# Kernel tuning notes

Hardware: AMD Instinct MI355X
Metric: run time of the kernel (lower is better)

Reference implementation:

```python
import jax, jax.numpy as jnp
import numpy as np

S = 2   # upsample scale
K = 5   # reassembly kernel k_up


def setup_inputs() -> dict:
    key = jax.random.key(0)
    ks = jax.random.split(key, 7)
    B, C, H, W = 4, 128, 64, 64
    C_MID = 64
    return {
        "x": jax.random.normal(ks[0], (B, C, H, W), dtype=jnp.float32),
        "w1": jax.random.normal(ks[1], (C_MID, C), dtype=jnp.float32) * 0.05,
        "w2": jax.random.normal(ks[2], (S * S * K * K, C_MID, 3, 3), dtype=jnp.float32) * 0.05,
        "bn_gamma": jax.random.uniform(ks[3], (C_MID,), dtype=jnp.float32, minval=0.5, maxval=1.5),
        "bn_beta": jax.random.normal(ks[4], (C_MID,), dtype=jnp.float32) * 0.1,
        "bn_mean": jax.random.normal(ks[5], (C_MID,), dtype=jnp.float32) * 0.1,
        "bn_var": jax.random.uniform(ks[6], (C_MID,), dtype=jnp.float32, minval=0.5, maxval=1.5),
    }


def reference(x, w1, w2, bn_gamma, bn_beta, bn_mean, bn_var):
    B, C, H, W = x.shape
    s, k = S, K
    eps = 1e-5
    # --- content encoder: 1x1 conv -> BN (inference form) -> ReLU -> 3x3 conv ---
    h = jnp.einsum('bchw,oc->bohw', x, w1)  # (B, c_mid, H, W)
    inv = bn_gamma / jnp.sqrt(bn_var + eps)
    h = h * inv[None, :, None, None] + (bn_beta - bn_mean * inv)[None, :, None, None]
    h = jax.nn.relu(h)
    ker = jax.lax.conv_general_dilated(
        h, w2, window_strides=(1, 1), padding=((1, 1), (1, 1)),
        dimension_numbers=('NCHW', 'OIHW', 'NCHW'))  # (B, s*s*k*k, H, W)
    # softmax over the k*k reassembly window
    ker = jax.nn.softmax(ker.reshape(B, s * s, k * k, H, W), axis=2)
    # --- unfold k x k neighborhoods of x (row-major window order, as F.unfold) ---
    p = k // 2
    xp = jnp.pad(x, ((0, 0), (0, 0), (p, p), (p, p)))
    patches = jnp.stack(
        [xp[:, :, i:i + H, j:j + W] for i in range(k) for j in range(k)],
        axis=2)  # (B, C, k*k, H, W)
    # weighted reassembly: sum over the k*k window per (sub-pixel, channel)
    out = jnp.einsum('bckhw,bskhw->bcshw', patches, ker)  # (B, C, s*s, H, W)
    # pixel shuffle: (B, C, s, s, H, W) -> (B, C, H*s, W*s)
    out = out.reshape(B, C, s, s, H, W).transpose(0, 1, 4, 2, 5, 3)
    return out.reshape(B, C, H * s, W * s)
```

## Files before the change

kernel.cpp:

```cpp
#include <hip/hip_runtime.h>
#include <hip/hip_bf16.h>

#define HW 4096

typedef __attribute__((ext_vector_type(8))) short  short8;
typedef __attribute__((ext_vector_type(4))) float  floatx4;

#define OFF_W2B 0ul
#define OFF_W1B 129024ul
#define OFF_BN  145408ul

__device__ __forceinline__ float bfbits(unsigned u) {
    union { unsigned u; float f; } t; t.u = u; return t.f;
}

__global__ __launch_bounds__(256) void prep_kernel(const float* __restrict__ w1,
                                                   const float* __restrict__ w2,
                                                   const float* __restrict__ gamma,
                                                   const float* __restrict__ beta,
                                                   const float* __restrict__ mean,
                                                   const float* __restrict__ var,
                                                   char* __restrict__ ws) {
    int tid = blockIdx.x * 256 + threadIdx.x;
    if (tid < 64512) {
        int n = tid / 576;
        int k = tid - n * 576;
        int t = k >> 6, c = k & 63;
        float v = (n < 100) ? w2[(n * 64 + c) * 9 + t] : 0.f;
        ((__hip_bfloat16*)(ws + OFF_W2B))[tid] = __float2bfloat16(v);
    } else if (tid < 64512 + 8192) {
        int i = tid - 64512;
        ((__hip_bfloat16*)(ws + OFF_W1B))[i] = __float2bfloat16(w1[i]);
    } else if (tid < 64512 + 8192 + 64) {
        int o = tid - 64512 - 8192;
        float inv = gamma[o] * rsqrtf(var[o] + 1e-5f);
        ((float2*)(ws + OFF_BN))[o] = make_float2(inv, beta[o] - mean[o] * inv);
    }
}

__global__ __launch_bounds__(1024, 8) void fused_carafe(const float* __restrict__ x,
                                                        const char* __restrict__ ws,
                                                        float* __restrict__ out) {
    __shared__ __align__(16) __hip_bfloat16 xs[96 * 136];
    __shared__ __align__(16) __hip_bfloat16 hs[60 * 72];
    __shared__ __align__(16) float lg[32 * 114];
    __shared__ __align__(16) float ks[32 * 104];

    int b    = blockIdx.x >> 7;
    int tile = blockIdx.x & 127;
    int ty0 = (tile >> 3) * 4;
    int tx0 = (tile & 7) * 8;
    int tid = threadIdx.x;
    int lane = tid & 63, wave = tid >> 6;
    int q = lane >> 4, m = lane & 15;

    int bnt = wave >> 2;
    int bo  = bnt * 16 + m;
    const __hip_bfloat16* w1b = (const __hip_bfloat16*)(ws + OFF_W1B);
    short8 bw[4];
    #pragma unroll
    for (int s = 0; s < 4; ++s)
        bw[s] = *(const short8*)(w1b + bo * 128 + s * 32 + q * 8);
    float2 bnia = ((const float2*)(ws + OFF_BN))[bo];

    const float* xb = x + (size_t)b * 128 * HW;
    #pragma unroll
    for (int i = 0; i < 12; ++i) {
        int idx = tid + i * 1024;
        int c = idx / 96, p = idx - c * 96;
        int hy = p / 12, hx = p - hy * 12;
        int gy = ty0 + hy - 2, gx = tx0 + hx - 2;
        float v = 0.f;
        if ((unsigned)gy < 64u && (unsigned)gx < 64u)
            v = xb[(size_t)c * HW + gy * 64 + gx];
        xs[p * 136 + c] = __float2bfloat16(v);
    }
    __syncthreads();

    {
        int mt = wave & 3;
        int hp = mt * 16 + m;
        int hy1 = hp / 10, hx1 = hp - hy1 * 10;
        int xrow = (hy1 + 1) * 12 + (hx1 + 1);
        floatx4 acc;
        #pragma unroll
        for (int r = 0; r < 4; ++r) acc[r] = 0.f;
        #pragma unroll
        for (int s = 0; s < 4; ++s) {
            short8 a = *(const short8*)(&xs[xrow * 136 + s * 32 + q * 8]);
            acc = __builtin_amdgcn_mfma_f32_16x16x32_bf16(a, bw[s], acc, 0, 0, 0);
        }
        #pragma unroll
        for (int r = 0; r < 4; ++r) {
            int prow = mt * 16 + q * 4 + r;
            if (prow < 60) {
                int phy = prow / 10, phx = prow - phy * 10;
                int gy = ty0 + phy - 1, gx = tx0 + phx - 1;
                bool in = ((unsigned)gy < 64u) && ((unsigned)gx < 64u);
                float v = in ? fmaxf(fmaf(acc[r], bnia.x, bnia.y), 0.f) : 0.f;
                hs[prow * 72 + bo] = __float2bfloat16(v);
            }
        }
    }
    __syncthreads();

    {
        int mt = wave & 1, nt = wave >> 1;
        if (nt < 7) {
            int pixidx = mt * 16 + m;
            int py = pixidx >> 3, px = pixidx & 7;
            const __hip_bfloat16* w2b = (const __hip_bfloat16*)(ws + OFF_W2B);
            const __hip_bfloat16* bp  = w2b + (size_t)(nt * 16 + m) * 576 + q * 8;

            floatx4 acc;
            #pragma unroll
            for (int r = 0; r < 4; ++r) acc[r] = 0.f;

            short8 bcur = *(const short8*)bp;
            for (int s = 0; s < 18; ++s) {
                int t = s >> 1, c0 = (s & 1) * 32;
                int ti = t / 3, tj = t - ti * 3;
                short8 a = *(const short8*)(&hs[((py + ti) * 10 + px + tj) * 72 + c0 + q * 8]);
                short8 bn2 = bcur;
                if (s < 17) bn2 = *(const short8*)(bp + (s + 1) * 32);
                acc = __builtin_amdgcn_mfma_f32_16x16x32_bf16(a, bcur, acc, 0, 0, 0);
                bcur = bn2;
            }
            #pragma unroll
            for (int r = 0; r < 4; ++r)
                lg[(mt * 16 + q * 4 + r) * 114 + nt * 16 + m] = acc[r];
        }
    }
    __syncthreads();

    if (tid < 128) {
        int pix = tid & 31, g = tid >> 5;
        float v[25];
        #pragma unroll
        for (int wi = 0; wi < 25; ++wi) v[wi] = lg[pix * 114 + g * 25 + wi];
        float mx = v[0];
        #pragma unroll
        for (int wi = 1; wi < 25; ++wi) mx = fmaxf(mx, v[wi]);
        float ssum = 0.f;
        #pragma unroll
        for (int wi = 0; wi < 25; ++wi) { v[wi] = __expf(v[wi] - mx); ssum += v[wi]; }
        float rs = 1.f / ssum;
        #pragma unroll
        for (int t25 = 0; t25 < 25; ++t25)
            ks[pix * 104 + t25 * 4 + g] = v[t25] * rs;
    }
    __syncthreads();

    {
        int pix   = lane & 31;
        int chsub = lane >> 5;
        int chb   = wave * 8 + chsub * 4;
        int py = pix >> 3, px = pix & 7;
        int Y = ty0 + py, X = tx0 + px;

        float acc[16];
        #pragma unroll
        for (int i = 0; i < 16; ++i) acc[i] = 0.f;

        #pragma unroll 5
        for (int t = 0; t < 25; ++t) {
            int ti = t / 5, tj = t - ti * 5;
            int xrow = (py + ti) * 12 + (px + tj);
            uint2 xv = *(const uint2*)(&xs[xrow * 136 + chb]);
            float4 kv = *(const float4*)(&ks[pix * 104 + t * 4]);
            float xf[4];
            xf[0] = bfbits(xv.x << 16);
            xf[1] = bfbits(xv.x & 0xFFFF0000u);
            xf[2] = bfbits(xv.y << 16);
            xf[3] = bfbits(xv.y & 0xFFFF0000u);
            #pragma unroll
            for (int i = 0; i < 4; ++i) {
                acc[i * 4 + 0] = fmaf(xf[i], kv.x, acc[i * 4 + 0]);
                acc[i * 4 + 1] = fmaf(xf[i], kv.y, acc[i * 4 + 1]);
                acc[i * 4 + 2] = fmaf(xf[i], kv.z, acc[i * 4 + 2]);
                acc[i * 4 + 3] = fmaf(xf[i], kv.w, acc[i * 4 + 3]);
            }
        }

        #pragma unroll
        for (int i = 0; i < 4; ++i) {
            size_t o0 = (((size_t)b * 128 + chb + i) * 128 + 2 * Y) * 128 + 2 * X;
            *(float2*)(out + o0)       = make_float2(acc[i * 4 + 0], acc[i * 4 + 1]);
            *(float2*)(out + o0 + 128) = make_float2(acc[i * 4 + 2], acc[i * 4 + 3]);
        }
    }
}

extern "C" void kernel_launch(void* const* d_in, const int* in_sizes, int n_in,
                              void* d_out, int out_size, void* d_ws, size_t ws_size,
                              hipStream_t stream) {
    const float* x     = (const float*)d_in[0];
    const float* w1    = (const float*)d_in[1];
    const float* w2    = (const float*)d_in[2];
    const float* gamma = (const float*)d_in[3];
    const float* beta  = (const float*)d_in[4];
    const float* mean  = (const float*)d_in[5];
    const float* var   = (const float*)d_in[6];
    float* out = (float*)d_out;
    char*  ws  = (char*)d_ws;

    prep_kernel<<<285, 256, 0, stream>>>(w1, w2, gamma, beta, mean, var, ws);
    fused_carafe<<<512, 1024, 0, stream>>>(x, ws, out);
}
```

Measured before the change: 108.8 us.

## Pre-convert x to bf16 channel-grouped layout in prep kernel for vector tile loads

The prep kernel now converts the full input x to bf16 in a [b][channel-group-of-8][pixel][8] layout in workspace. The main kernel loads its halo tile with 16-byte vector loads instead of scalar strided fp32 loads, and the shared tile becomes channel-group-major. The reassembly stage is remapped so each wave handles 8 channels and one output sub-row, with a transposed softmax-weight layout to avoid bank conflicts. This trades an extra full pass over x (read fp32, write bf16) on every call for cheaper, coalesced tile loads in the fused kernel.

```diff
diff --git a/kernel.cpp b/kernel.cpp
--- a/kernel.cpp
+++ b/kernel.cpp
@@ -9,12 +9,14 @@
 #define OFF_W2B 0ul
 #define OFF_W1B 129024ul
 #define OFF_BN  145408ul
+#define OFF_XG  145920ul
 
 __device__ __forceinline__ float bfbits(unsigned u) {
     union { unsigned u; float f; } t; t.u = u; return t.f;
 }
 
-__global__ __launch_bounds__(256) void prep_kernel(const float* __restrict__ w1,
+__global__ __launch_bounds__(256) void prep_kernel(const float* __restrict__ x,
+                                                   const float* __restrict__ w1,
                                                    const float* __restrict__ w2,
                                                    const float* __restrict__ gamma,
                                                    const float* __restrict__ beta,
@@ -22,29 +24,40 @@
                                                    const float* __restrict__ var,
                                                    char* __restrict__ ws) {
     int tid = blockIdx.x * 256 + threadIdx.x;
-    if (tid < 64512) {
-        int n = tid / 576;
-        int k = tid - n * 576;
+    if (tid < 262144) {
+        int pix = tid & 4095;
+        int cq  = (tid >> 12) & 15;
+        int b   = tid >> 16;
+        const float* xp = x + ((size_t)(b * 128 + cq * 8)) * HW + pix;
+        union { short8 s; __hip_bfloat16 h[8]; } u;
+        #pragma unroll
+        for (int cc = 0; cc < 8; ++cc) u.h[cc] = __float2bfloat16(xp[(size_t)cc * HW]);
+        *(short8*)((__hip_bfloat16*)(ws + OFF_XG) + (size_t)tid * 8) = u.s;
+        return;
+    }
+    int t2 = tid - 262144;
+    if (t2 < 64512) {
+        int n = t2 / 576;
+        int k = t2 - n * 576;
         int t = k >> 6, c = k & 63;
         float v = (n < 100) ? w2[(n * 64 + c) * 9 + t] : 0.f;
-        ((__hip_bfloat16*)(ws + OFF_W2B))[tid] = __float2bfloat16(v);
-    } else if (tid < 64512 + 8192) {
-        int i = tid - 64512;
+        ((__hip_bfloat16*)(ws + OFF_W2B))[t2] = __float2bfloat16(v);
+    } else if (t2 < 64512 + 8192) {
+        int i = t2 - 64512;
         ((__hip_bfloat16*)(ws + OFF_W1B))[i] = __float2bfloat16(w1[i]);
-    } else if (tid < 64512 + 8192 + 64) {
-        int o = tid - 64512 - 8192;
+    } else if (t2 < 64512 + 8192 + 64) {
+        int o = t2 - 64512 - 8192;
         float inv = gamma[o] * rsqrtf(var[o] + 1e-5f);
         ((float2*)(ws + OFF_BN))[o] = make_float2(inv, beta[o] - mean[o] * inv);
     }
 }
 
-__global__ __launch_bounds__(1024, 8) void fused_carafe(const float* __restrict__ x,
-                                                        const char* __restrict__ ws,
+__global__ __launch_bounds__(1024, 8) void fused_carafe(const char* __restrict__ ws,
                                                         float* __restrict__ out) {
-    __shared__ __align__(16) __hip_bfloat16 xs[96 * 136];
+    __shared__ __align__(16) __hip_bfloat16 xs[1536 * 8];
     __shared__ __align__(16) __hip_bfloat16 hs[60 * 72];
     __shared__ __align__(16) float lg[32 * 114];
-    __shared__ __align__(16) float ks[32 * 104];
+    __shared__ __align__(16) float ks[100 * 33];
 
     int b    = blockIdx.x >> 7;
     int tile = blockIdx.x & 127;
@@ -63,17 +76,21 @@
         bw[s] = *(const short8*)(w1b + bo * 128 + s * 32 + q * 8);
     float2 bnia = ((const float2*)(ws + OFF_BN))[bo];
 
-    const float* xb = x + (size_t)b * 128 * HW;
+    const __hip_bfloat16* xg = (const __hip_bfloat16*)(ws + OFF_XG) + (size_t)b * 16 * 4096 * 8;
     #pragma unroll
-    for (int i = 0; i < 12; ++i) {
-        int idx = tid + i * 1024;
-        int c = idx / 96, p = idx - c * 96;
-        int hy = p / 12, hx = p - hy * 12;
-        int gy = ty0 + hy - 2, gx = tx0 + hx - 2;
-        float v = 0.f;
-        if ((unsigned)gy < 64u && (unsigned)gx < 64u)
-            v = xb[(size_t)c * HW + gy * 64 + gx];
-        xs[p * 136 + c] = __float2bfloat16(v);
+    for (int it = 0; it < 2; ++it) {
+        int idx = tid + it * 1024;
+        if (idx < 1536) {
+            int cq = idx / 96, p = idx - cq * 96;
+            int hy = p / 12, hx = p - hy * 12;
+            int gy = ty0 + hy - 2, gx = tx0 + hx - 2;
+            short8 v;
+            #pragma unroll
+            for (int j = 0; j < 8; ++j) v[j] = 0;
+            if ((unsigned)gy < 64u && (unsigned)gx < 64u)
+                v = *(const short8*)(xg + ((size_t)cq * 4096 + gy * 64 + gx) * 8);
+            *(short8*)(&xs[idx * 8]) = v;
+        }
     }
     __syncthreads();
 
@@ -87,7 +104,7 @@
         for (int r = 0; r < 4; ++r) acc[r] = 0.f;
         #pragma unroll
         for (int s = 0; s < 4; ++s) {
-            short8 a = *(const short8*)(&xs[xrow * 136 + s * 32 + q * 8]);
+            short8 a = *(const short8*)(&xs[((s * 4 + q) * 96 + xrow) * 8]);
             acc = __builtin_amdgcn_mfma_f32_16x16x32_bf16(a, bw[s], acc, 0, 0, 0);
         }
         #pragma unroll
@@ -147,14 +164,14 @@
         float rs = 1.f / ssum;
         #pragma unroll
         for (int t25 = 0; t25 < 25; ++t25)
-            ks[pix * 104 + t25 * 4 + g] = v[t25] * rs;
+            ks[(t25 * 4 + g) * 33 + pix] = v[t25] * rs;
     }
     __syncthreads();
 
     {
         int pix   = lane & 31;
-        int chsub = lane >> 5;
-        int chb   = wave * 8 + chsub * 4;
+        int chunk = lane >> 5;
+        int co    = wave;
         int py = pix >> 3, px = pix & 7;
         int Y = ty0 + py, X = tx0 + px;
 
@@ -162,31 +179,30 @@
         #pragma unroll
         for (int i = 0; i < 16; ++i) acc[i] = 0.f;
 
+        const __hip_bfloat16* xsb = xs + (size_t)co * 96 * 8;
         #pragma unroll 5
         for (int t = 0; t < 25; ++t) {
             int ti = t / 5, tj = t - ti * 5;
             int xrow = (py + ti) * 12 + (px + tj);
-            uint2 xv = *(const uint2*)(&xs[xrow * 136 + chb]);
-            float4 kv = *(const float4*)(&ks[pix * 104 + t * 4]);
-            float xf[4];
-            xf[0] = bfbits(xv.x << 16);
-            xf[1] = bfbits(xv.x & 0xFFFF0000u);
-            xf[2] = bfbits(xv.y << 16);
-            xf[3] = bfbits(xv.y & 0xFFFF0000u);
-            #pragma unroll
-            for (int i = 0; i < 4; ++i) {
-                acc[i * 4 + 0] = fmaf(xf[i], kv.x, acc[i * 4 + 0]);
-                acc[i * 4 + 1] = fmaf(xf[i], kv.y, acc[i * 4 + 1]);
-                acc[i * 4 + 2] = fmaf(xf[i], kv.z, acc[i * 4 + 2]);
-                acc[i * 4 + 3] = fmaf(xf[i], kv.w, acc[i * 4 + 3]);
+            union { short8 s; unsigned u[4]; } xv;
+            xv.s = *(const short8*)(xsb + xrow * 8);
+            float k0 = ks[(t * 4 + chunk * 2 + 0) * 33 + pix];
+            float k1 = ks[(t * 4 + chunk * 2 + 1) * 33 + pix];
+            #pragma unroll
+            for (int j = 0; j < 4; ++j) {
+                float xa = bfbits(xv.u[j] << 16);
+                float xb2 = bfbits(xv.u[j] & 0xFFFF0000u);
+                acc[(j * 2 + 0) * 2 + 0] = fmaf(xa,  k0, acc[(j * 2 + 0) * 2 + 0]);
+                acc[(j * 2 + 0) * 2 + 1] = fmaf(xa,  k1, acc[(j * 2 + 0) * 2 + 1]);
+                acc[(j * 2 + 1) * 2 + 0] = fmaf(xb2, k0, acc[(j * 2 + 1) * 2 + 0]);
+                acc[(j * 2 + 1) * 2 + 1] = fmaf(xb2, k1, acc[(j * 2 + 1) * 2 + 1]);
             }
         }
 
         #pragma unroll
-        for (int i = 0; i < 4; ++i) {
-            size_t o0 = (((size_t)b * 128 + chb + i) * 128 + 2 * Y) * 128 + 2 * X;
-            *(float2*)(out + o0)       = make_float2(acc[i * 4 + 0], acc[i * 4 + 1]);
-            *(float2*)(out + o0 + 128) = make_float2(acc[i * 4 + 2], acc[i * 4 + 3]);
+        for (int i = 0; i < 8; ++i) {
+            size_t o0 = (((size_t)b * 128 + co * 8 + i) * 128 + 2 * Y + chunk) * 128 + 2 * X;
+            *(float2*)(out + o0) = make_float2(acc[i * 2 + 0], acc[i * 2 + 1]);
         }
     }
 }
@@ -204,6 +220,6 @@
     float* out = (float*)d_out;
     char*  ws  = (char*)d_ws;
 
-    prep_kernel<<<285, 256, 0, stream>>>(w1, w2, gamma, beta, mean, var, ws);
-    fused_carafe<<<512, 1024, 0, stream>>>(x, ws, out);
-}
+    prep_kernel<<<1309, 256, 0, stream>>>(x, w1, w2, gamma, beta, mean, var, ws);
+    fused_carafe<<<512, 1024, 0, stream>>>(ws, out);
+}
```

Result: faster. 105.9 us (-2.7%).
